# Performance work log

Measured on AMD Instinct MI355X. Metric: run time of the kernel, lower is better.

Reference implementation:

```python
import jax, jax.numpy as jnp
import numpy as np

N, E, D, H = 50000, 800000, 128, 8
DH = D // H
EPS = 1e-12


def setup_inputs() -> dict:
    key = jax.random.key(0)
    ks = jax.random.split(key, 12)
    s = 0.02
    return {
        "h": jax.random.normal(ks[0], (N, D), jnp.float32),
        "Wq": jax.random.normal(ks[1], (D, D), jnp.float32) * s,
        "bq": jax.random.normal(ks[2], (D,), jnp.float32) * s,
        "Wk": jax.random.normal(ks[3], (D, D), jnp.float32) * s,
        "bk": jax.random.normal(ks[4], (D,), jnp.float32) * s,
        "Wv": jax.random.normal(ks[5], (D, D), jnp.float32) * s,
        "bv": jax.random.normal(ks[6], (D,), jnp.float32) * s,
        "Wo": jax.random.normal(ks[7], (D, D), jnp.float32) * s,
        "bo": jax.random.normal(ks[8], (D,), jnp.float32) * s,
        "gamma": jnp.ones((D,), jnp.float32),
        "beta": jnp.zeros((D,), jnp.float32),
        "src": jax.random.randint(ks[9], (E,), 0, N, jnp.int32),
        "dst": jax.random.randint(ks[10], (E,), 0, N, jnp.int32),
    }


def reference(h, Wq, bq, Wk, bk, Wv, bv, Wo, bo, gamma, beta, src, dst):
    n = h.shape[0]
    # node-wise projections, split into heads: [N, H, DH]
    Q = (h @ Wq + bq).reshape(n, H, DH)
    K = (h @ Wk + bk).reshape(n, H, DH)
    V = (h @ Wv + bv).reshape(n, H, DH)
    # edge-wise scores: sum over head dim of K[src] * Q[dst] -> [E, H]
    scores = jnp.sum(K[src] * Q[dst], axis=-1)
    # edge softmax, normalized over incoming edges of each dst node
    m = jax.lax.stop_gradient(jax.ops.segment_max(scores, dst, num_segments=n))
    ex = jnp.exp(scores - m[dst])
    denom = jax.ops.segment_sum(ex, dst, num_segments=n)
    p = ex / denom[dst]  # [E, H]
    # weighted message + scatter-sum aggregate -> [N, H, DH]
    msg = V[src] * p[:, :, None]
    agg = jax.ops.segment_sum(msg, dst, num_segments=n).reshape(n, D)
    # BertSelfOutput: dense + residual + layernorm (dropout is identity in eval)
    y = agg @ Wo + bo + h
    mu = jnp.mean(y, axis=-1, keepdims=True)
    var = jnp.mean(jnp.square(y - mu), axis=-1, keepdims=True)
    out = (y - mu) / jnp.sqrt(var + EPS) * gamma + beta
    return out
```

## Files before the change

kernel.cpp:

```cpp
#include <hip/hip_runtime.h>
#include <hip/hip_bf16.h>
#include <math.h>

#define D 128
#define EPS 1e-12f

typedef __attribute__((ext_vector_type(8))) short bf16x8;
typedef __attribute__((ext_vector_type(4))) float f32x4;
typedef __attribute__((ext_vector_type(2))) float f32x2;

__device__ __forceinline__ unsigned short f2bf(float f) {
    unsigned int u = __float_as_uint(f);
    return (unsigned short)((u + 0x7fffu + ((u >> 16) & 1u)) >> 16);
}
__device__ __forceinline__ float bf2f_lo(unsigned int packed) {
    return __uint_as_float(packed << 16);
}
__device__ __forceinline__ float bf2f_hi(unsigned int packed) {
    return __uint_as_float(packed & 0xffff0000u);
}
__device__ __forceinline__ unsigned char f2fp8(float f) {
    return (unsigned char)__builtin_amdgcn_cvt_pk_fp8_f32(f, f, 0, false);
}

__global__ __launch_bounds__(256) void prep_kernel(
    const float* __restrict__ Wq, const float* __restrict__ Wk,
    const float* __restrict__ Wv, const float* __restrict__ Wo,
    unsigned short* __restrict__ WT,
    const int* __restrict__ dst, int* __restrict__ counts,
    int* __restrict__ ticket, int E) {
    int bx = blockIdx.x;
    int tid = threadIdx.x;
    if (bx < 64) {
        __shared__ unsigned short tile[32][33];
        int m = bx >> 4;
        int t = bx & 15;
        const float* W = (m == 0) ? Wq : (m == 1) ? Wk : (m == 2) ? Wv : Wo;
        int r0 = (t & 3) * 32;
        int c0 = (t >> 2) * 32;
        int row = tid >> 3, c4 = (tid & 7) * 4;
        float4 v = *(const float4*)&W[(size_t)(r0 + row) * D + c0 + c4];
        tile[c4 + 0][row] = f2bf(v.x);
        tile[c4 + 1][row] = f2bf(v.y);
        tile[c4 + 2][row] = f2bf(v.z);
        tile[c4 + 3][row] = f2bf(v.w);
        __syncthreads();
        unsigned int lo = (unsigned int)tile[row][c4] | ((unsigned int)tile[row][c4 + 1] << 16);
        unsigned int hi = (unsigned int)tile[row][c4 + 2] | ((unsigned int)tile[row][c4 + 3] << 16);
        uint2 pk; pk.x = lo; pk.y = hi;
        int n = c0 + row;
        int ct = n >> 4, l15 = n & 15;
        int ks = t & 3;
        int quad = c4 >> 3;
        int j = c4 & 7;
        size_t off = (size_t)m * 16384 + (size_t)(((ct * 4 + ks) * 64) + quad * 16 + l15) * 8 + j;
        *(uint2*)&WT[off] = pk;
    } else {
        int e = ((bx - 64) * 256 + tid) * 4;
        if (e >= E) return;
        if (e + 3 < E) {
            int4 d4 = *(const int4*)&dst[e];
            int4 t4;
            t4.x = atomicAdd(&counts[d4.x], 1);
            t4.y = atomicAdd(&counts[d4.y], 1);
            t4.z = atomicAdd(&counts[d4.z], 1);
            t4.w = atomicAdd(&counts[d4.w], 1);
            *(int4*)&ticket[e] = t4;
        } else {
            for (int i = e; i < E; ++i) ticket[i] = atomicAdd(&counts[dst[i]], 1);
        }
    }
}

__device__ __forceinline__ int block_incl_scan256(int v, int tid, int* wsum) {
    int lane = tid & 63;
    int wid = tid >> 6;
#pragma unroll
    for (int off = 1; off < 64; off <<= 1) {
        int t = __shfl_up(v, off, 64);
        if (lane >= off) v += t;
    }
    if (lane == 63) wsum[wid] = v;
    __syncthreads();
#pragma unroll
    for (int w = 0; w < 4; ++w)
        if (w < wid) v += wsum[w];
    return v;
}

__global__ void scan1_kernel(const int* __restrict__ counts, int* __restrict__ offsets,
                             int* __restrict__ chunksum, int n) {
    __shared__ int wsum[4];
    int tid = threadIdx.x;
    int i = blockIdx.x * 256 + tid;
    int v = (i < n) ? counts[i] : 0;
    int incl = block_incl_scan256(v, tid, wsum);
    if (i < n) offsets[i + 1] = incl;
    if (tid == 255) chunksum[blockIdx.x] = incl;
}

__global__ void scan2_kernel(const int* __restrict__ chunksum, int* __restrict__ chunkbase, int nchunks) {
    __shared__ int wsum[4];
    int tid = threadIdx.x;
    int v = (tid < nchunks) ? chunksum[tid] : 0;
    int incl = block_incl_scan256(v, tid, wsum);
    if (tid < nchunks) chunkbase[tid] = incl - v;
}

__global__ void scan3_kernel(int* __restrict__ offsets, const int* __restrict__ chunkbase, int n) {
    int i = blockIdx.x * 256 + threadIdx.x;
    if (i < n) {
        offsets[i + 1] += chunkbase[blockIdx.x];
        if (i == 0) offsets[0] = 0;
    }
}

__global__ void fill_kernel(const int* __restrict__ dst, const int* __restrict__ src,
                            const int* __restrict__ ticket, const int* __restrict__ offsets,
                            int* __restrict__ psrc, int E) {
    int e = (blockIdx.x * 256 + threadIdx.x) * 4;
    if (e >= E) return;
    if (e + 3 < E) {
        int4 d4 = *(const int4*)&dst[e];
        int4 s4 = *(const int4*)&src[e];
        int4 t4 = *(const int4*)&ticket[e];
        psrc[offsets[d4.x] + t4.x] = s4.x;
        psrc[offsets[d4.y] + t4.y] = s4.y;
        psrc[offsets[d4.z] + t4.z] = s4.z;
        psrc[offsets[d4.w] + t4.w] = s4.w;
    } else {
        for (int i = e; i < E; ++i) psrc[offsets[dst[i]] + ticket[i]] = src[i];
    }
}

__global__ __launch_bounds__(256) void qkv_mfma_kernel(
    const float* __restrict__ h, const unsigned short* __restrict__ WT,
    const float* __restrict__ bq, const float* __restrict__ bk, const float* __restrict__ bv,
    unsigned short* __restrict__ Qb, unsigned char* __restrict__ K8,
    unsigned char* __restrict__ V8, int n) {
    __shared__ __align__(16) unsigned short wt[16384];
    int tid = threadIdx.x;
    int lane = tid & 63, wave = tid >> 6;
    int quad = lane >> 4, l15 = lane & 15;
    int rt = blockIdx.x * 64 + wave * 16;

    int rowA = min(rt + l15, n - 1);
    bf16x8 af[4];
#pragma unroll
    for (int ks = 0; ks < 4; ++ks) {
        const float* ap = &h[(size_t)rowA * D + ks * 32 + quad * 8];
        float4 a0 = *(const float4*)ap;
        float4 a1 = *(const float4*)(ap + 4);
        union { unsigned short u[8]; bf16x8 v; } pk;
        pk.u[0] = f2bf(a0.x); pk.u[1] = f2bf(a0.y);
        pk.u[2] = f2bf(a0.z); pk.u[3] = f2bf(a0.w);
        pk.u[4] = f2bf(a1.x); pk.u[5] = f2bf(a1.y);
        pk.u[6] = f2bf(a1.z); pk.u[7] = f2bf(a1.w);
        af[ks] = pk.v;
    }

    for (int m = 0; m < 3; ++m) {
#pragma unroll
        for (int it = 0; it < 8; ++it) {
            int idx = it * 256 + tid;
            *(uint4*)&wt[idx * 8] = *(const uint4*)&WT[(size_t)m * 16384 + idx * 8];
        }
        __syncthreads();

        f32x4 acc[8];
#pragma unroll
        for (int ct = 0; ct < 8; ++ct) {
            acc[ct] = (f32x4){0.f, 0.f, 0.f, 0.f};
#pragma unroll
            for (int ks = 0; ks < 4; ++ks) {
                bf16x8 bfr = *(const bf16x8*)&wt[((ct * 4 + ks) * 64 + lane) * 8];
                acc[ct] = __builtin_amdgcn_mfma_f32_16x16x32_bf16(af[ks], bfr, acc[ct], 0, 0, 0);
            }
        }
        __syncthreads();

        const float* bias = (m == 0) ? bq : (m == 1) ? bk : bv;
#pragma unroll
        for (int ct = 0; ct < 8; ++ct) {
            int col = ct * 16 + l15;
            float bb = bias[col];
#pragma unroll
            for (int r = 0; r < 4; ++r) {
                int row = rt + quad * 4 + r;
                if (row < n) {
                    float v = acc[ct][r] + bb;
                    if (m == 0)      Qb[(size_t)row * D + col] = f2bf(v);
                    else if (m == 1) K8[(size_t)row * D + col] = f2fp8(v);
                    else             V8[(size_t)row * D + col] = f2fp8(v);
                }
            }
        }
    }
}

__global__ __launch_bounds__(256) void edge_attn_kernel(
    const unsigned short* __restrict__ Qb, const unsigned char* __restrict__ K8,
    const unsigned char* __restrict__ V8,
    const int* __restrict__ offsets, const int* __restrict__ psrc,
    unsigned short* __restrict__ aggb, int n) {
    int wave = (blockIdx.x * 256 + threadIdx.x) >> 6;
    int lane = threadIdx.x & 63;
    if (wave >= n) return;
    int start = offsets[wave], end = offsets[wave + 1];
    int j = lane >> 3, hd = lane & 7;

    const unsigned short* qp = &Qb[(size_t)wave * D + hd * 16];
    uint4 qa = *(const uint4*)qp;
    uint4 qb = *(const uint4*)(qp + 8);
    float q[16];
    q[0] = bf2f_lo(qa.x);  q[1] = bf2f_hi(qa.x);
    q[2] = bf2f_lo(qa.y);  q[3] = bf2f_hi(qa.y);
    q[4] = bf2f_lo(qa.z);  q[5] = bf2f_hi(qa.z);
    q[6] = bf2f_lo(qa.w);  q[7] = bf2f_hi(qa.w);
    q[8] = bf2f_lo(qb.x);  q[9] = bf2f_hi(qb.x);
    q[10] = bf2f_lo(qb.y); q[11] = bf2f_hi(qb.y);
    q[12] = bf2f_lo(qb.z); q[13] = bf2f_hi(qb.z);
    q[14] = bf2f_lo(qb.w); q[15] = bf2f_hi(qb.w);

    float l = 0.f;
    float acc[16] = {};

    if (start < end) {
        int s = psrc[min(start + j, end - 1)];
        for (int base = start; base < end; base += 8) {
            uint4 ku = *(const uint4*)&K8[(size_t)s * D + hd * 16];
            uint4 vu = *(const uint4*)&V8[(size_t)s * D + hd * 16];
            int nb = base + 8;
            int sn = (nb < end) ? psrc[min(nb + j, end - 1)] : 0;
            bool valid = (base + j) < end;

            float kf[16], vf[16];
            {
                f32x2 t;
                t = __builtin_amdgcn_cvt_pk_f32_fp8(ku.x, false); kf[0] = t.x;  kf[1] = t.y;
                t = __builtin_amdgcn_cvt_pk_f32_fp8(ku.x, true);  kf[2] = t.x;  kf[3] = t.y;
                t = __builtin_amdgcn_cvt_pk_f32_fp8(ku.y, false); kf[4] = t.x;  kf[5] = t.y;
                t = __builtin_amdgcn_cvt_pk_f32_fp8(ku.y, true);  kf[6] = t.x;  kf[7] = t.y;
                t = __builtin_amdgcn_cvt_pk_f32_fp8(ku.z, false); kf[8] = t.x;  kf[9] = t.y;
                t = __builtin_amdgcn_cvt_pk_f32_fp8(ku.z, true);  kf[10] = t.x; kf[11] = t.y;
                t = __builtin_amdgcn_cvt_pk_f32_fp8(ku.w, false); kf[12] = t.x; kf[13] = t.y;
                t = __builtin_amdgcn_cvt_pk_f32_fp8(ku.w, true);  kf[14] = t.x; kf[15] = t.y;
                t = __builtin_amdgcn_cvt_pk_f32_fp8(vu.x, false); vf[0] = t.x;  vf[1] = t.y;
                t = __builtin_amdgcn_cvt_pk_f32_fp8(vu.x, true);  vf[2] = t.x;  vf[3] = t.y;
                t = __builtin_amdgcn_cvt_pk_f32_fp8(vu.y, false); vf[4] = t.x;  vf[5] = t.y;
                t = __builtin_amdgcn_cvt_pk_f32_fp8(vu.y, true);  vf[6] = t.x;  vf[7] = t.y;
                t = __builtin_amdgcn_cvt_pk_f32_fp8(vu.z, false); vf[8] = t.x;  vf[9] = t.y;
                t = __builtin_amdgcn_cvt_pk_f32_fp8(vu.z, true);  vf[10] = t.x; vf[11] = t.y;
                t = __builtin_amdgcn_cvt_pk_f32_fp8(vu.w, false); vf[12] = t.x; vf[13] = t.y;
                t = __builtin_amdgcn_cvt_pk_f32_fp8(vu.w, true);  vf[14] = t.x; vf[15] = t.y;
            }

            float sc = q[0] * kf[0];
#pragma unroll
            for (int i = 1; i < 16; ++i) sc = fmaf(q[i], kf[i], sc);

            float p = valid ? __expf(sc) : 0.f;
            l += p;
#pragma unroll
            for (int i = 0; i < 16; ++i) acc[i] = fmaf(p, vf[i], acc[i]);
            s = sn;
        }
    }

#pragma unroll
    for (int off = 8; off <= 32; off <<= 1) {
        l += __shfl_xor(l, off, 64);
#pragma unroll
        for (int i = 0; i < 16; ++i) acc[i] += __shfl_xor(acc[i], off, 64);
    }
    float inv = (l > 0.f) ? 1.f / l : 0.f;
    if (j == 0) {
        uint4 o0, o1;
        o0.x = (unsigned int)f2bf(acc[0] * inv) | ((unsigned int)f2bf(acc[1] * inv) << 16);
        o0.y = (unsigned int)f2bf(acc[2] * inv) | ((unsigned int)f2bf(acc[3] * inv) << 16);
        o0.z = (unsigned int)f2bf(acc[4] * inv) | ((unsigned int)f2bf(acc[5] * inv) << 16);
        o0.w = (unsigned int)f2bf(acc[6] * inv) | ((unsigned int)f2bf(acc[7] * inv) << 16);
        o1.x = (unsigned int)f2bf(acc[8] * inv) | ((unsigned int)f2bf(acc[9] * inv) << 16);
        o1.y = (unsigned int)f2bf(acc[10] * inv) | ((unsigned int)f2bf(acc[11] * inv) << 16);
        o1.z = (unsigned int)f2bf(acc[12] * inv) | ((unsigned int)f2bf(acc[13] * inv) << 16);
        o1.w = (unsigned int)f2bf(acc[14] * inv) | ((unsigned int)f2bf(acc[15] * inv) << 16);
        unsigned short* op = &aggb[(size_t)wave * D + hd * 16];
        *(uint4*)op = o0;
        *(uint4*)(op + 8) = o1;
    }
}

__global__ __launch_bounds__(256) void out_ln_mfma_kernel(
    const unsigned short* __restrict__ aggb, const unsigned short* __restrict__ WTo,
    const float* __restrict__ bo, const float* __restrict__ hres,
    const float* __restrict__ gamma, const float* __restrict__ beta,
    float* __restrict__ out, int n) {
    int tid = threadIdx.x;
    int lane = tid & 63, wave = tid >> 6;
    int quad = lane >> 4, l15 = lane & 15;
    int rt = blockIdx.x * 64 + wave * 16;

    int rowA = min(rt + l15, n - 1);
    bf16x8 af[4];
#pragma unroll
    for (int ks = 0; ks < 4; ++ks)
        af[ks] = *(const bf16x8*)&aggb[(size_t)rowA * D + ks * 32 + quad * 8];

    f32x4 acc[8];
#pragma unroll
    for (int ct = 0; ct < 8; ++ct) {
        acc[ct] = (f32x4){0.f, 0.f, 0.f, 0.f};
#pragma unroll
        for (int ks = 0; ks < 4; ++ks) {
            bf16x8 bfr = *(const bf16x8*)&WTo[(size_t)((ct * 4 + ks) * 64 + lane) * 8];
            acc[ct] = __builtin_amdgcn_mfma_f32_16x16x32_bf16(af[ks], bfr, acc[ct], 0, 0, 0);
        }
    }

    float bb[8], gg[8], be[8];
#pragma unroll
    for (int ct = 0; ct < 8; ++ct) {
        int col = ct * 16 + l15;
        bb[ct] = bo[col];
        gg[ct] = gamma[col];
        be[ct] = beta[col];
    }
#pragma unroll
    for (int ct = 0; ct < 8; ++ct) {
        int col = ct * 16 + l15;
#pragma unroll
        for (int r = 0; r < 4; ++r) {
            int row = rt + quad * 4 + r;
            float hv = (row < n) ? hres[(size_t)row * D + col] : 0.f;
            acc[ct][r] = acc[ct][r] + bb[ct] + hv;
        }
    }

#pragma unroll
    for (int r = 0; r < 4; ++r) {
        float s1 = 0.f, s2 = 0.f;
#pragma unroll
        for (int ct = 0; ct < 8; ++ct) {
            float v = acc[ct][r];
            s1 += v;
            s2 += v * v;
        }
        s1 += __shfl_xor(s1, 1, 64); s2 += __shfl_xor(s2, 1, 64);
        s1 += __shfl_xor(s1, 2, 64); s2 += __shfl_xor(s2, 2, 64);
        s1 += __shfl_xor(s1, 4, 64); s2 += __shfl_xor(s2, 4, 64);
        s1 += __shfl_xor(s1, 8, 64); s2 += __shfl_xor(s2, 8, 64);
        float mu = s1 * (1.f / 128.f);
        float var = s2 * (1.f / 128.f) - mu * mu;
        float rs = rsqrtf(fmaxf(var, 0.f) + EPS);
        int row = rt + quad * 4 + r;
        if (row < n) {
#pragma unroll
            for (int ct = 0; ct < 8; ++ct) {
                int col = ct * 16 + l15;
                out[(size_t)row * D + col] = (acc[ct][r] - mu) * rs * gg[ct] + be[ct];
            }
        }
    }
}

extern "C" void kernel_launch(void* const* d_in, const int* in_sizes, int n_in,
                              void* d_out, int out_size, void* d_ws, size_t ws_size,
                              hipStream_t stream) {
    const float* h     = (const float*)d_in[0];
    const float* Wq    = (const float*)d_in[1];
    const float* bq    = (const float*)d_in[2];
    const float* Wk    = (const float*)d_in[3];
    const float* bk    = (const float*)d_in[4];
    const float* Wv    = (const float*)d_in[5];
    const float* bv    = (const float*)d_in[6];
    const float* Wo    = (const float*)d_in[7];
    const float* bo    = (const float*)d_in[8];
    const float* gamma = (const float*)d_in[9];
    const float* beta  = (const float*)d_in[10];
    const int* src     = (const int*)d_in[11];
    const int* dst     = (const int*)d_in[12];
    float* out = (float*)d_out;

    int N = in_sizes[0] / D;
    int E = in_sizes[11];

    unsigned short* Qb = (unsigned short*)d_ws;
    unsigned short* Ab = Qb + (size_t)N * D;
    unsigned short* WT = Ab + (size_t)N * D;
    unsigned char* K8  = (unsigned char*)(WT + 4 * D * D);
    unsigned char* V8  = K8 + (size_t)N * D;
    int* counts   = (int*)(V8 + (size_t)N * D);
    int* offsets  = counts + N;
    int* chunksum = offsets + (N + 1);
    int* chunkbase = chunksum + 256;
    int* ticket   = chunkbase + 256;
    int* psrc     = ticket + E;

    int nchunks = (N + 255) / 256;
    int e4blocks = ((E + 3) / 4 + 255) / 256;

    hipMemsetAsync(counts, 0, (size_t)N * sizeof(int), stream);
    prep_kernel<<<64 + e4blocks, 256, 0, stream>>>(Wq, Wk, Wv, Wo, WT, dst, counts, ticket, E);
    scan1_kernel<<<nchunks, 256, 0, stream>>>(counts, offsets, chunksum, N);
    scan2_kernel<<<1, 256, 0, stream>>>(chunksum, chunkbase, nchunks);
    scan3_kernel<<<nchunks, 256, 0, stream>>>(offsets, chunkbase, N);
    fill_kernel<<<e4blocks, 256, 0, stream>>>(dst, src, ticket, offsets, psrc, E);
    qkv_mfma_kernel<<<(N + 63) / 64, 256, 0, stream>>>(h, WT, bq, bk, bv, Qb, K8, V8, N);
    edge_attn_kernel<<<(N + 3) / 4, 256, 0, stream>>>(Qb, K8, V8, offsets, psrc, Ab, N);
    out_ln_mfma_kernel<<<(N + 63) / 64, 256, 0, stream>>>(Ab, WT + 3 * D * D, bo, h, gamma, beta, out, N);
}
```

Before: 229.7 us.

## Fuse CSR fill into QKV kernel and split edge attention across two waves per node

The psrc fill pass and the QKV projection are merged into one launch, with the first blocks doing the scatter and the rest doing the MFMA projection, which removes a launch and lets the two independent jobs overlap. Edge attention now uses two waves per node, each covering four heads, with 16 edges in flight per iteration instead of 8. This doubles the wave count and the per-node parallelism, aimed at latency-bound gathers. The cost is a longer shuffle reduction, and the fused kernel's fill blocks still reserve the large shared-memory array, which can limit occupancy.

```diff
diff --git a/kernel.cpp b/kernel.cpp
--- a/kernel.cpp
+++ b/kernel.cpp
@@ -115,34 +115,37 @@
     }
 }
 
-__global__ void fill_kernel(const int* __restrict__ dst, const int* __restrict__ src,
-                            const int* __restrict__ ticket, const int* __restrict__ offsets,
-                            int* __restrict__ psrc, int E) {
-    int e = (blockIdx.x * 256 + threadIdx.x) * 4;
-    if (e >= E) return;
-    if (e + 3 < E) {
-        int4 d4 = *(const int4*)&dst[e];
-        int4 s4 = *(const int4*)&src[e];
-        int4 t4 = *(const int4*)&ticket[e];
-        psrc[offsets[d4.x] + t4.x] = s4.x;
-        psrc[offsets[d4.y] + t4.y] = s4.y;
-        psrc[offsets[d4.z] + t4.z] = s4.z;
-        psrc[offsets[d4.w] + t4.w] = s4.w;
-    } else {
-        for (int i = e; i < E; ++i) psrc[offsets[dst[i]] + ticket[i]] = src[i];
-    }
-}
-
-__global__ __launch_bounds__(256) void qkv_mfma_kernel(
+__global__ __launch_bounds__(256) void fill_qkv_kernel(
+    const int* __restrict__ dst, const int* __restrict__ src,
+    const int* __restrict__ ticket, const int* __restrict__ offsets,
+    int* __restrict__ psrc, int E, int e4blocks,
     const float* __restrict__ h, const unsigned short* __restrict__ WT,
     const float* __restrict__ bq, const float* __restrict__ bk, const float* __restrict__ bv,
     unsigned short* __restrict__ Qb, unsigned char* __restrict__ K8,
     unsigned char* __restrict__ V8, int n) {
     __shared__ __align__(16) unsigned short wt[16384];
+    int bx = blockIdx.x;
     int tid = threadIdx.x;
+    if (bx < e4blocks) {
+        int e = (bx * 256 + tid) * 4;
+        if (e >= E) return;
+        if (e + 3 < E) {
+            int4 d4 = *(const int4*)&dst[e];
+            int4 s4 = *(const int4*)&src[e];
+            int4 t4 = *(const int4*)&ticket[e];
+            psrc[offsets[d4.x] + t4.x] = s4.x;
+            psrc[offsets[d4.y] + t4.y] = s4.y;
+            psrc[offsets[d4.z] + t4.z] = s4.z;
+            psrc[offsets[d4.w] + t4.w] = s4.w;
+        } else {
+            for (int i = e; i < E; ++i) psrc[offsets[dst[i]] + ticket[i]] = src[i];
+        }
+        return;
+    }
+    int bid = bx - e4blocks;
     int lane = tid & 63, wave = tid >> 6;
     int quad = lane >> 4, l15 = lane & 15;
-    int rt = blockIdx.x * 64 + wave * 16;
+    int rt = bid * 64 + wave * 16;
 
     int rowA = min(rt + l15, n - 1);
     bf16x8 af[4];
@@ -203,13 +206,15 @@
     const unsigned char* __restrict__ V8,
     const int* __restrict__ offsets, const int* __restrict__ psrc,
     unsigned short* __restrict__ aggb, int n) {
-    int wave = (blockIdx.x * 256 + threadIdx.x) >> 6;
+    int gw = (blockIdx.x * 256 + threadIdx.x) >> 6;
+    int node = gw >> 1, half = gw & 1;
     int lane = threadIdx.x & 63;
-    if (wave >= n) return;
-    int start = offsets[wave], end = offsets[wave + 1];
-    int j = lane >> 3, hd = lane & 7;
-
-    const unsigned short* qp = &Qb[(size_t)wave * D + hd * 16];
+    if (node >= n) return;
+    int start = offsets[node], end = offsets[node + 1];
+    int j = lane >> 2, hd4 = lane & 3;
+    int head = half * 4 + hd4;
+
+    const unsigned short* qp = &Qb[(size_t)node * D + head * 16];
     uint4 qa = *(const uint4*)qp;
     uint4 qb = *(const uint4*)(qp + 8);
     float q[16];
@@ -227,10 +232,10 @@
 
     if (start < end) {
         int s = psrc[min(start + j, end - 1)];
-        for (int base = start; base < end; base += 8) {
-            uint4 ku = *(const uint4*)&K8[(size_t)s * D + hd * 16];
-            uint4 vu = *(const uint4*)&V8[(size_t)s * D + hd * 16];
-            int nb = base + 8;
+        for (int base = start; base < end; base += 16) {
+            uint4 ku = *(const uint4*)&K8[(size_t)s * D + head * 16];
+            uint4 vu = *(const uint4*)&V8[(size_t)s * D + head * 16];
+            int nb = base + 16;
             int sn = (nb < end) ? psrc[min(nb + j, end - 1)] : 0;
             bool valid = (base + j) < end;
 
@@ -268,7 +273,7 @@
     }
 
 #pragma unroll
-    for (int off = 8; off <= 32; off <<= 1) {
+    for (int off = 4; off <= 32; off <<= 1) {
         l += __shfl_xor(l, off, 64);
 #pragma unroll
         for (int i = 0; i < 16; ++i) acc[i] += __shfl_xor(acc[i], off, 64);
@@ -284,7 +289,7 @@
         o1.y = (unsigned int)f2bf(acc[10] * inv) | ((unsigned int)f2bf(acc[11] * inv) << 16);
         o1.z = (unsigned int)f2bf(acc[12] * inv) | ((unsigned int)f2bf(acc[13] * inv) << 16);
         o1.w = (unsigned int)f2bf(acc[14] * inv) | ((unsigned int)f2bf(acc[15] * inv) << 16);
-        unsigned short* op = &aggb[(size_t)wave * D + hd * 16];
+        unsigned short* op = &aggb[(size_t)node * D + head * 16];
         *(uint4*)op = o0;
         *(uint4*)(op + 8) = o1;
     }
@@ -398,14 +403,16 @@
 
     int nchunks = (N + 255) / 256;
     int e4blocks = ((E + 3) / 4 + 255) / 256;
+    int nqkv = (N + 63) / 64;
 
     hipMemsetAsync(counts, 0, (size_t)N * sizeof(int), stream);
     prep_kernel<<<64 + e4blocks, 256, 0, stream>>>(Wq, Wk, Wv, Wo, WT, dst, counts, ticket, E);
     scan1_kernel<<<nchunks, 256, 0, stream>>>(counts, offsets, chunksum, N);
     scan2_kernel<<<1, 256, 0, stream>>>(chunksum, chunkbase, nchunks);
     scan3_kernel<<<nchunks, 256, 0, stream>>>(offsets, chunkbase, N);
-    fill_kernel<<<e4blocks, 256, 0, stream>>>(dst, src, ticket, offsets, psrc, E);
-    qkv_mfma_kernel<<<(N + 63) / 64, 256, 0, stream>>>(h, WT, bq, bk, bv, Qb, K8, V8, N);
-    edge_attn_kernel<<<(N + 3) / 4, 256, 0, stream>>>(Qb, K8, V8, offsets, psrc, Ab, N);
+    fill_qkv_kernel<<<e4blocks + nqkv, 256, 0, stream>>>(
+        dst, src, ticket, offsets, psrc, E, e4blocks,
+        h, WT, bq, bk, bv, Qb, K8, V8, N);
+    edge_attn_kernel<<<(2 * N + 3) / 4, 256, 0, stream>>>(Qb, K8, V8, offsets, psrc, Ab, N);
     out_ln_mfma_kernel<<<(N + 63) / 64, 256, 0, stream>>>(Ab, WT + 3 * D * D, bo, h, gamma, beta, out, N);
 }
```

After: 264.3 us. 15.1% more time.

## Co-schedule ticket atomics with QKV projection and prefetch next K/V in edge loop

Applied to the files above, without the earlier changes.

Splits weight conversion into its own small kernel and merges the per-edge ticket atomic counting with the QKV MFMA projection into one launch. Separate blocks do each job, so the latency-bound atomics overlap with the compute-bound GEMM. The ticket blocks now handle one edge per thread rather than four, and every block of the merged kernel reserves the 32 KB LDS buffer, which may limit how many atomic blocks can run at once. Separately, the edge attention loop now issues the K/V loads for the next batch of 8 edges before it computes the current one, hiding gather latency at the cost of extra registers.

```diff
diff --git a/kernel.cpp b/kernel.cpp
--- a/kernel.cpp
+++ b/kernel.cpp
@@ -23,51 +23,107 @@
     return (unsigned char)__builtin_amdgcn_cvt_pk_fp8_f32(f, f, 0, false);
 }
 
-__global__ __launch_bounds__(256) void prep_kernel(
+__global__ __launch_bounds__(256) void wconv_kernel(
     const float* __restrict__ Wq, const float* __restrict__ Wk,
     const float* __restrict__ Wv, const float* __restrict__ Wo,
-    unsigned short* __restrict__ WT,
-    const int* __restrict__ dst, int* __restrict__ counts,
-    int* __restrict__ ticket, int E) {
+    unsigned short* __restrict__ WT) {
+    __shared__ unsigned short tile[32][33];
     int bx = blockIdx.x;
     int tid = threadIdx.x;
-    if (bx < 64) {
-        __shared__ unsigned short tile[32][33];
-        int m = bx >> 4;
-        int t = bx & 15;
-        const float* W = (m == 0) ? Wq : (m == 1) ? Wk : (m == 2) ? Wv : Wo;
-        int r0 = (t & 3) * 32;
-        int c0 = (t >> 2) * 32;
-        int row = tid >> 3, c4 = (tid & 7) * 4;
-        float4 v = *(const float4*)&W[(size_t)(r0 + row) * D + c0 + c4];
-        tile[c4 + 0][row] = f2bf(v.x);
-        tile[c4 + 1][row] = f2bf(v.y);
-        tile[c4 + 2][row] = f2bf(v.z);
-        tile[c4 + 3][row] = f2bf(v.w);
+    int m = bx >> 4;
+    int t = bx & 15;
+    const float* W = (m == 0) ? Wq : (m == 1) ? Wk : (m == 2) ? Wv : Wo;
+    int r0 = (t & 3) * 32;
+    int c0 = (t >> 2) * 32;
+    int row = tid >> 3, c4 = (tid & 7) * 4;
+    float4 v = *(const float4*)&W[(size_t)(r0 + row) * D + c0 + c4];
+    tile[c4 + 0][row] = f2bf(v.x);
+    tile[c4 + 1][row] = f2bf(v.y);
+    tile[c4 + 2][row] = f2bf(v.z);
+    tile[c4 + 3][row] = f2bf(v.w);
+    __syncthreads();
+    unsigned int lo = (unsigned int)tile[row][c4] | ((unsigned int)tile[row][c4 + 1] << 16);
+    unsigned int hi = (unsigned int)tile[row][c4 + 2] | ((unsigned int)tile[row][c4 + 3] << 16);
+    uint2 pk; pk.x = lo; pk.y = hi;
+    int n = c0 + row;
+    int ct = n >> 4, l15 = n & 15;
+    int ks = t & 3;
+    int quad = c4 >> 3;
+    int j = c4 & 7;
+    size_t off = (size_t)m * 16384 + (size_t)(((ct * 4 + ks) * 64) + quad * 16 + l15) * 8 + j;
+    *(uint2*)&WT[off] = pk;
+}
+
+__global__ __launch_bounds__(256) void ticket_qkv_kernel(
+    const int* __restrict__ dst, int* __restrict__ counts,
+    int* __restrict__ ticket, int E, int tblocks,
+    const float* __restrict__ h, const unsigned short* __restrict__ WT,
+    const float* __restrict__ bq, const float* __restrict__ bk, const float* __restrict__ bv,
+    unsigned short* __restrict__ Qb, unsigned char* __restrict__ K8,
+    unsigned char* __restrict__ V8, int n) {
+    __shared__ __align__(16) unsigned short wt[16384];
+    int bx = blockIdx.x;
+    int tid = threadIdx.x;
+    if (bx < tblocks) {
+        int e = bx * 256 + tid;
+        if (e < E) ticket[e] = atomicAdd(&counts[dst[e]], 1);
+        return;
+    }
+    int bid = bx - tblocks;
+    int lane = tid & 63, wave = tid >> 6;
+    int quad = lane >> 4, l15 = lane & 15;
+    int rt = bid * 64 + wave * 16;
+
+    int rowA = min(rt + l15, n - 1);
+    bf16x8 af[4];
+#pragma unroll
+    for (int ks = 0; ks < 4; ++ks) {
+        const float* ap = &h[(size_t)rowA * D + ks * 32 + quad * 8];
+        float4 a0 = *(const float4*)ap;
+        float4 a1 = *(const float4*)(ap + 4);
+        union { unsigned short u[8]; bf16x8 v; } pk;
+        pk.u[0] = f2bf(a0.x); pk.u[1] = f2bf(a0.y);
+        pk.u[2] = f2bf(a0.z); pk.u[3] = f2bf(a0.w);
+        pk.u[4] = f2bf(a1.x); pk.u[5] = f2bf(a1.y);
+        pk.u[6] = f2bf(a1.z); pk.u[7] = f2bf(a1.w);
+        af[ks] = pk.v;
+    }
+
+    for (int m = 0; m < 3; ++m) {
+#pragma unroll
+        for (int it = 0; it < 8; ++it) {
+            int idx = it * 256 + tid;
+            *(uint4*)&wt[idx * 8] = *(const uint4*)&WT[(size_t)m * 16384 + idx * 8];
+        }
         __syncthreads();
-        unsigned int lo = (unsigned int)tile[row][c4] | ((unsigned int)tile[row][c4 + 1] << 16);
-        unsigned int hi = (unsigned int)tile[row][c4 + 2] | ((unsigned int)tile[row][c4 + 3] << 16);
-        uint2 pk; pk.x = lo; pk.y = hi;
-        int n = c0 + row;
-        int ct = n >> 4, l15 = n & 15;
-        int ks = t & 3;
-        int quad = c4 >> 3;
-        int j = c4 & 7;
-        size_t off = (size_t)m * 16384 + (size_t)(((ct * 4 + ks) * 64) + quad * 16 + l15) * 8 + j;
-        *(uint2*)&WT[off] = pk;
-    } else {
-        int e = ((bx - 64) * 256 + tid) * 4;
-        if (e >= E) return;
-        if (e + 3 < E) {
-            int4 d4 = *(const int4*)&dst[e];
-            int4 t4;
-            t4.x = atomicAdd(&counts[d4.x], 1);
-            t4.y = atomicAdd(&counts[d4.y], 1);
-            t4.z = atomicAdd(&counts[d4.z], 1);
-            t4.w = atomicAdd(&counts[d4.w], 1);
-            *(int4*)&ticket[e] = t4;
-        } else {
-            for (int i = e; i < E; ++i) ticket[i] = atomicAdd(&counts[dst[i]], 1);
+
+        f32x4 acc[8];
+#pragma unroll
+        for (int ct = 0; ct < 8; ++ct) {
+            acc[ct] = (f32x4){0.f, 0.f, 0.f, 0.f};
+#pragma unroll
+            for (int ks = 0; ks < 4; ++ks) {
+                bf16x8 bfr = *(const bf16x8*)&wt[((ct * 4 + ks) * 64 + lane) * 8];
+                acc[ct] = __builtin_amdgcn_mfma_f32_16x16x32_bf16(af[ks], bfr, acc[ct], 0, 0, 0);
+            }
+        }
+        __syncthreads();
+
+        const float* bias = (m == 0) ? bq : (m == 1) ? bk : bv;
+#pragma unroll
+        for (int ct = 0; ct < 8; ++ct) {
+            int col = ct * 16 + l15;
+            float bb = bias[col];
+#pragma unroll
+            for (int r = 0; r < 4; ++r) {
+                int row = rt + quad * 4 + r;
+                if (row < n) {
+                    float v = acc[ct][r] + bb;
+                    if (m == 0)      Qb[(size_t)row * D + col] = f2bf(v);
+                    else if (m == 1) K8[(size_t)row * D + col] = f2fp8(v);
+                    else             V8[(size_t)row * D + col] = f2fp8(v);
+                }
+            }
         }
     }
 }
@@ -133,71 +189,6 @@
     }
 }
 
-__global__ __launch_bounds__(256) void qkv_mfma_kernel(
-    const float* __restrict__ h, const unsigned short* __restrict__ WT,
-    const float* __restrict__ bq, const float* __restrict__ bk, const float* __restrict__ bv,
-    unsigned short* __restrict__ Qb, unsigned char* __restrict__ K8,
-    unsigned char* __restrict__ V8, int n) {
-    __shared__ __align__(16) unsigned short wt[16384];
-    int tid = threadIdx.x;
-    int lane = tid & 63, wave = tid >> 6;
-    int quad = lane >> 4, l15 = lane & 15;
-    int rt = blockIdx.x * 64 + wave * 16;
-
-    int rowA = min(rt + l15, n - 1);
-    bf16x8 af[4];
-#pragma unroll
-    for (int ks = 0; ks < 4; ++ks) {
-        const float* ap = &h[(size_t)rowA * D + ks * 32 + quad * 8];
-        float4 a0 = *(const float4*)ap;
-        float4 a1 = *(const float4*)(ap + 4);
-        union { unsigned short u[8]; bf16x8 v; } pk;
-        pk.u[0] = f2bf(a0.x); pk.u[1] = f2bf(a0.y);
-        pk.u[2] = f2bf(a0.z); pk.u[3] = f2bf(a0.w);
-        pk.u[4] = f2bf(a1.x); pk.u[5] = f2bf(a1.y);
-        pk.u[6] = f2bf(a1.z); pk.u[7] = f2bf(a1.w);
-        af[ks] = pk.v;
-    }
-
-    for (int m = 0; m < 3; ++m) {
-#pragma unroll
-        for (int it = 0; it < 8; ++it) {
-            int idx = it * 256 + tid;
-            *(uint4*)&wt[idx * 8] = *(const uint4*)&WT[(size_t)m * 16384 + idx * 8];
-        }
-        __syncthreads();
-
-        f32x4 acc[8];
-#pragma unroll
-        for (int ct = 0; ct < 8; ++ct) {
-            acc[ct] = (f32x4){0.f, 0.f, 0.f, 0.f};
-#pragma unroll
-            for (int ks = 0; ks < 4; ++ks) {
-                bf16x8 bfr = *(const bf16x8*)&wt[((ct * 4 + ks) * 64 + lane) * 8];
-                acc[ct] = __builtin_amdgcn_mfma_f32_16x16x32_bf16(af[ks], bfr, acc[ct], 0, 0, 0);
-            }
-        }
-        __syncthreads();
-
-        const float* bias = (m == 0) ? bq : (m == 1) ? bk : bv;
-#pragma unroll
-        for (int ct = 0; ct < 8; ++ct) {
-            int col = ct * 16 + l15;
-            float bb = bias[col];
-#pragma unroll
-            for (int r = 0; r < 4; ++r) {
-                int row = rt + quad * 4 + r;
-                if (row < n) {
-                    float v = acc[ct][r] + bb;
-                    if (m == 0)      Qb[(size_t)row * D + col] = f2bf(v);
-                    else if (m == 1) K8[(size_t)row * D + col] = f2fp8(v);
-                    else             V8[(size_t)row * D + col] = f2fp8(v);
-                }
-            }
-        }
-    }
-}
-
 __global__ __launch_bounds__(256) void edge_attn_kernel(
     const unsigned short* __restrict__ Qb, const unsigned char* __restrict__ K8,
     const unsigned char* __restrict__ V8,
@@ -227,11 +218,13 @@
 
     if (start < end) {
         int s = psrc[min(start + j, end - 1)];
+        uint4 ku = *(const uint4*)&K8[(size_t)s * D + hd * 16];
+        uint4 vu = *(const uint4*)&V8[(size_t)s * D + hd * 16];
         for (int base = start; base < end; base += 8) {
-            uint4 ku = *(const uint4*)&K8[(size_t)s * D + hd * 16];
-            uint4 vu = *(const uint4*)&V8[(size_t)s * D + hd * 16];
             int nb = base + 8;
             int sn = (nb < end) ? psrc[min(nb + j, end - 1)] : 0;
+            uint4 kun = *(const uint4*)&K8[(size_t)sn * D + hd * 16];
+            uint4 vun = *(const uint4*)&V8[(size_t)sn * D + hd * 16];
             bool valid = (base + j) < end;
 
             float kf[16], vf[16];
@@ -263,7 +256,7 @@
             l += p;
 #pragma unroll
             for (int i = 0; i < 16; ++i) acc[i] = fmaf(p, vf[i], acc[i]);
-            s = sn;
+            ku = kun; vu = vun; s = sn;
         }
     }
 
@@ -398,14 +391,18 @@
 
     int nchunks = (N + 255) / 256;
     int e4blocks = ((E + 3) / 4 + 255) / 256;
+    int tblocks = (E + 255) / 256;
+    int nqkv = (N + 63) / 64;
 
     hipMemsetAsync(counts, 0, (size_t)N * sizeof(int), stream);
-    prep_kernel<<<64 + e4blocks, 256, 0, stream>>>(Wq, Wk, Wv, Wo, WT, dst, counts, ticket, E);
+    wconv_kernel<<<64, 256, 0, stream>>>(Wq, Wk, Wv, Wo, WT);
+    ticket_qkv_kernel<<<tblocks + nqkv, 256, 0, stream>>>(
+        dst, counts, ticket, E, tblocks,
+        h, WT, bq, bk, bv, Qb, K8, V8, N);
     scan1_kernel<<<nchunks, 256, 0, stream>>>(counts, offsets, chunksum, N);
     scan2_kernel<<<1, 256, 0, stream>>>(chunksum, chunkbase, nchunks);
     scan3_kernel<<<nchunks, 256, 0, stream>>>(offsets, chunkbase, N);
     fill_kernel<<<e4blocks, 256, 0, stream>>>(dst, src, ticket, offsets, psrc, E);
-    qkv_mfma_kernel<<<(N + 63) / 64, 256, 0, stream>>>(h, WT, bq, bk, bv, Qb, K8, V8, N);
     edge_attn_kernel<<<(N + 3) / 4, 256, 0, stream>>>(Qb, K8, V8, offsets, psrc, Ab, N);
     out_ln_mfma_kernel<<<(N + 63) / 64, 256, 0, stream>>>(Ab, WT + 3 * D * D, bo, h, gamma, beta, out, N);
 }
```

After: 227.6 us. No clear change (-0.9%).
